# Optimization experiments

Hardware: AMD Instinct MI355X
Metric: run time of the kernel (lower is better)

## Reference

```python
import math
import jax, jax.numpy as jnp
import numpy as np

B, S, D, H, FF = 2, 2048, 1024, 16, 4096
DH = D // H
NUM_BUCKETS, MAX_DISTANCE = 32, 128
EPS_LN = 1e-5


def setup_inputs() -> dict:
    key = jax.random.key(0)
    ks = jax.random.split(key, 12)
    sc = 0.02
    return {
        "x": jax.random.normal(ks[0], (B, S, D), dtype=jnp.float32),
        "Wq": jax.random.normal(ks[1], (D, D), dtype=jnp.float32) * sc,
        "bq": jnp.zeros((D,), jnp.float32),
        "Wk": jax.random.normal(ks[2], (D, D), dtype=jnp.float32) * sc,
        "bk": jnp.zeros((D,), jnp.float32),
        "Wv": jax.random.normal(ks[3], (D, D), dtype=jnp.float32) * sc,
        "bv": jnp.zeros((D,), jnp.float32),
        "Wo": jax.random.normal(ks[4], (D, D), dtype=jnp.float32) * sc,
        "bo": jnp.zeros((D,), jnp.float32),
        "W1": jax.random.normal(ks[5], (D, FF), dtype=jnp.float32) * sc,
        "b1": jnp.zeros((FF,), jnp.float32),
        "W2": jax.random.normal(ks[6], (FF, D), dtype=jnp.float32) * sc,
        "b2": jnp.zeros((D,), jnp.float32),
        "g1": jnp.ones((D,), jnp.float32),
        "beta1": jnp.zeros((D,), jnp.float32),
        "g2": jnp.ones((D,), jnp.float32),
        "beta2": jnp.zeros((D,), jnp.float32),
        "rel_emb": jax.random.normal(ks[7], (NUM_BUCKETS, H), dtype=jnp.float32) * sc,
        "pad_mask": jnp.ones((B, 1, 1, S), dtype=jnp.bool_),
    }


def _rel_bias(rel_emb, qlen, klen):
    # T5 bidirectional relative position bucketing; n = q_pos - k_pos
    q = jnp.arange(qlen)[:, None]
    k = jnp.arange(klen)[None, :]
    n = q - k
    half = NUM_BUCKETS // 2           # 16
    ret = (n < 0).astype(jnp.int32) * half
    n_abs = jnp.abs(n)
    max_exact = half // 2             # 8
    log_ratio = math.log(MAX_DISTANCE / max_exact)
    val_large = (max_exact + jnp.log(n_abs.astype(jnp.float32) / max_exact + 1e-6)
                 / log_ratio * (half - max_exact)).astype(jnp.int32)
    val_large = jnp.minimum(val_large, half - 1)
    bucket = jnp.where(n_abs < max_exact, n_abs.astype(jnp.int32), val_large) + ret
    bias = rel_emb[bucket]            # [Q, K, H]
    return jnp.transpose(bias, (2, 0, 1))[None]  # [1, H, Q, K]


def _layernorm(x, g, b):
    mu = jnp.mean(x, axis=-1, keepdims=True)
    var = jnp.mean(jnp.square(x - mu), axis=-1, keepdims=True)
    return (x - mu) * jax.lax.rsqrt(var + EPS_LN) * g + b


def reference(x, Wq, bq, Wk, bk, Wv, bv, Wo, bo, W1, b1, W2, b2,
              g1, beta1, g2, beta2, rel_emb, pad_mask):
    b_, s_, d_ = x.shape
    rel = _rel_bias(rel_emb, s_, s_)
    h = _layernorm(x, g1, beta1)
    q = (h @ Wq + bq).reshape(b_, s_, H, DH)
    k = (h @ Wk + bk).reshape(b_, s_, H, DH)
    v = (h @ Wv + bv).reshape(b_, s_, H, DH)
    scores = jnp.einsum("bqhd,bkhd->bhqk", q, k) / math.sqrt(DH)
    scores = scores + rel
    scores = jnp.where(pad_mask, scores, jnp.finfo(scores.dtype).min)
    attn = jax.nn.softmax(scores, axis=-1)
    out = jnp.einsum("bhqk,bkhd->bqhd", attn, v).reshape(b_, s_, d_)
    x = x + (out @ Wo + bo)
    h2 = _layernorm(x, g2, beta2)
    ff = jax.nn.gelu(h2 @ W1 + b1, approximate=False) @ W2 + b2
    return x + ff
```

## Files before the change

kernel.cpp:

```cpp
#include <hip/hip_runtime.h>
#include <hip/hip_bf16.h>
#include <math.h>

#define S_LEN 2048
#define DMODEL 1024
#define NHEAD 16
#define FFDIM 4096
#define NTOK 4096
#define QKV_LD 3072

typedef __attribute__((ext_vector_type(8))) short bf16x8;
typedef __attribute__((ext_vector_type(4))) float f32x4;

static __device__ __forceinline__ unsigned short f2bf_bits(float f) {
    union { __hip_bfloat16 b; unsigned short u; } cv;
    cv.b = __float2bfloat16(f);
    return cv.u;
}

#define GLOAD16(src, dst) \
    __builtin_amdgcn_global_load_lds((const __attribute__((address_space(1))) void*)(src), \
                                     (__attribute__((address_space(3))) void*)(dst), 16, 0, 0)

__global__ __launch_bounds__(256) void transpose_bf16(
    const float* __restrict__ in, __hip_bfloat16* __restrict__ out, int R, int C)
{
    __shared__ float tile[32][33];
    const int c0 = blockIdx.x * 32, r0 = blockIdx.y * 32;
    const int tx = threadIdx.x & 31, ty = threadIdx.x >> 5;
#pragma unroll
    for (int i = 0; i < 4; i++) {
        int r = ty + i * 8;
        tile[r][tx] = in[(long)(r0 + r) * C + c0 + tx];
    }
    __syncthreads();
#pragma unroll
    for (int i = 0; i < 4; i++) {
        int c = ty + i * 8;
        out[(long)(c0 + c) * R + r0 + tx] = __float2bfloat16(tile[tx][c]);
    }
}

__global__ __launch_bounds__(256) void transpose_qkv_v(
    const __hip_bfloat16* __restrict__ in,
    __hip_bfloat16* __restrict__ out)
{
    __shared__ __hip_bfloat16 tile[32][33];
    const int bz = blockIdx.z;
    const int c0 = blockIdx.x * 32, r0 = blockIdx.y * 32;
    const int tx = threadIdx.x & 31, ty = threadIdx.x >> 5;
    const long ibase = (long)bz * S_LEN * QKV_LD;
#pragma unroll
    for (int i = 0; i < 4; i++) {
        int r = ty + i * 8;
        tile[r][tx] = in[ibase + (long)(r0 + r) * QKV_LD + c0 + tx];
    }
    __syncthreads();
    const long obase = (long)bz * DMODEL * S_LEN;
#pragma unroll
    for (int i = 0; i < 4; i++) {
        int c = ty + i * 8;
        out[obase + (long)(c0 + c) * S_LEN + r0 + tx] = tile[tx][c];
    }
}

__global__ __launch_bounds__(256) void biastab_kernel(
    const float* __restrict__ rel_emb, float* __restrict__ tab)
{
    int i = blockIdx.x * 256 + threadIdx.x;
    int h = i >> 12, idx = i & 4095;
    if (h >= NHEAD || idx >= 4095) return;
    int n = idx - 2047;
    int ret = (n < 0) ? 16 : 0;
    int na = (n < 0) ? -n : n;
    int bucket;
    if (na < 8) {
        bucket = na;
    } else {
        float vv = 8.0f + logf((float)na * 0.125f + 1e-6f) * (8.0f / 2.7725887222397811f);
        int vi = (int)vv;
        bucket = (vi < 15) ? vi : 15;
    }
    bucket += ret;
    tab[h * 4096 + idx] = rel_emb[bucket * NHEAD + h];
}

__global__ __launch_bounds__(256) void ln_bf16(
    const float* __restrict__ x, const float* __restrict__ gm,
    const float* __restrict__ bt, __hip_bfloat16* __restrict__ out)
{
    const long row = blockIdx.x;
    const int tid = threadIdx.x, w = tid >> 6;
    float4 v = ((const float4*)(x + row * DMODEL))[tid];
    float s = v.x + v.y + v.z + v.w;
#pragma unroll
    for (int m = 32; m >= 1; m >>= 1) s += __shfl_xor(s, m);
    __shared__ float red[4], red2[4];
    if ((tid & 63) == 0) red[w] = s;
    __syncthreads();
    float mu = (red[0] + red[1] + red[2] + red[3]) * (1.0f / DMODEL);
    float dx = v.x - mu, dy = v.y - mu, dz = v.z - mu, dw = v.w - mu;
    float s2 = dx * dx + dy * dy + dz * dz + dw * dw;
#pragma unroll
    for (int m = 32; m >= 1; m >>= 1) s2 += __shfl_xor(s2, m);
    if ((tid & 63) == 0) red2[w] = s2;
    __syncthreads();
    float var = (red2[0] + red2[1] + red2[2] + red2[3]) * (1.0f / DMODEL);
    float rs = rsqrtf(var + 1e-5f);
    float4 g4 = ((const float4*)gm)[tid];
    float4 b4 = ((const float4*)bt)[tid];
    long o = row * DMODEL + tid * 4;
    out[o + 0] = __float2bfloat16(dx * rs * g4.x + b4.x);
    out[o + 1] = __float2bfloat16(dy * rs * g4.y + b4.y);
    out[o + 2] = __float2bfloat16(dz * rs * g4.z + b4.z);
    out[o + 3] = __float2bfloat16(dw * rs * g4.w + b4.w);
}

template<int EPI>
__global__ __launch_bounds__(256) void gemm_bt(
    const __hip_bfloat16* __restrict__ A,
    const __hip_bfloat16* __restrict__ Bt,
    const float* __restrict__ bias,
    const float* __restrict__ resid,
    float* __restrict__ outf,
    __hip_bfloat16* __restrict__ outb,
    int K, int N)
{
    __shared__ __hip_bfloat16 As[2][128 * 32];
    __shared__ __hip_bfloat16 Bs[2][128 * 32];
    const int tid = threadIdx.x;
    const int lane = tid & 63, w = tid >> 6;
    const int cl = lane & 15, g = lane >> 4;
    const int wr = w >> 1, wc = w & 1;
    const int bm = blockIdx.x, bn = blockIdx.y;

    f32x4 acc[4][4] = {};

    const __hip_bfloat16* agp0 = A + (long)(bm * 128 + (tid >> 2)) * K + (tid & 3) * 8;
    const __hip_bfloat16* agp1 = agp0 + (long)64 * K;
    const __hip_bfloat16* bgp0 = Bt + (long)(bn * 128 + (tid >> 2)) * K + (tid & 3) * 8;
    const __hip_bfloat16* bgp1 = bgp0 + (long)64 * K;

    auto STAGE = [&](int buf, int k0) {
        GLOAD16(agp0 + k0, (char*)&As[buf][0] + w * 1024);
        GLOAD16(agp1 + k0, (char*)&As[buf][0] + 4096 + w * 1024);
        GLOAD16(bgp0 + k0, (char*)&Bs[buf][0] + w * 1024);
        GLOAD16(bgp1 + k0, (char*)&Bs[buf][0] + 4096 + w * 1024);
    };

    STAGE(0, 0);
    asm volatile("s_waitcnt vmcnt(0)" ::: "memory");
    __builtin_amdgcn_s_barrier();

    int cur = 0;
    for (int k0 = 0; k0 < K; k0 += 32) {
        if (k0 + 32 < K) STAGE(cur ^ 1, k0 + 32);
        bf16x8 af[4], bfv[4];
#pragma unroll
        for (int m = 0; m < 4; m++)
            af[m] = *reinterpret_cast<const bf16x8*>(&As[cur][(wr * 64 + m * 16 + cl) * 32 + g * 8]);
#pragma unroll
        for (int n = 0; n < 4; n++)
            bfv[n] = *reinterpret_cast<const bf16x8*>(&Bs[cur][(wc * 64 + n * 16 + cl) * 32 + g * 8]);
        __builtin_amdgcn_s_setprio(1);
#pragma unroll
        for (int m = 0; m < 4; m++)
#pragma unroll
            for (int n = 0; n < 4; n++)
                acc[m][n] = __builtin_amdgcn_mfma_f32_16x16x32_bf16(af[m], bfv[n], acc[m][n], 0, 0, 0);
        __builtin_amdgcn_s_setprio(0);
        asm volatile("s_waitcnt vmcnt(0)" ::: "memory");
        __builtin_amdgcn_s_barrier();
        cur ^= 1;
    }

#pragma unroll
    for (int m = 0; m < 4; m++) {
#pragma unroll
        for (int n = 0; n < 4; n++) {
#pragma unroll
            for (int r = 0; r < 4; r++) {
                int row = bm * 128 + wr * 64 + m * 16 + g * 4 + r;
                int col = bn * 128 + wc * 64 + n * 16 + cl;
                float vv = acc[m][n][r] + bias[col];
                long off = (long)row * N + col;
                if (EPI == 1) {
                    outf[off] = vv + resid[off];
                } else {
                    outb[off] = __float2bfloat16(vv);
                }
            }
        }
    }
}

template<int EPI>
__global__ __launch_bounds__(512, 2) void gemm256(
    const __hip_bfloat16* __restrict__ A,
    const __hip_bfloat16* __restrict__ Bt,
    const float* __restrict__ bias,
    const float* __restrict__ bias2,
    const float* __restrict__ bias3,
    __hip_bfloat16* __restrict__ outb,
    int K, int N)
{
    __shared__ char L[131072];
    const int tid = threadIdx.x, lane = tid & 63, w = tid >> 6;
    const int cl = lane & 15, g = lane >> 4;
    const int wm = w >> 2, wn = w & 3;
    const int nbn = N >> 8;
    const int nwg = 16 * nbn;
    const int bid = blockIdx.x;
    const int swz = (bid & 7) * (nwg >> 3) + (bid >> 3);
    const int bm = swz / nbn, bn = swz - bm * nbn;
    const int NT = K >> 6;

    f32x4 acc[8][4] = {};

    const int srow = tid >> 3;
    const int scol = ((tid & 7) ^ (srow & 7)) * 8;
    const __hip_bfloat16* Asrc = A  + (long)(bm * 256 + srow) * K + scol;
    const __hip_bfloat16* Bsrc = Bt + (long)(bn * 256 + srow) * K + scol;

    auto STAGE_A = [&](int buf, int half, int t) {
        const __hip_bfloat16* s = Asrc + (long)(half * 128) * K + t * 64;
        char* d = L + buf * 32768 + half * 16384 + w * 1024;
        GLOAD16(s, d);
        GLOAD16(s + (long)64 * K, d + 8192);
    };
    auto STAGE_B = [&](int buf, int half, int t) {
        const __hip_bfloat16* s = Bsrc + (long)(half * 128) * K + t * 64;
        char* d = L + 65536 + buf * 32768 + half * 16384 + w * 1024;
        GLOAD16(s, d);
        GLOAD16(s + (long)64 * K, d + 8192);
    };

    const char* arb = L + wm * 16384 + cl * 128;
    const char* brb = L + 65536 + (wn >> 1) * 16384 + (((wn & 1) * 64 + cl)) * 128;
    const int xo0 = (g * 16) ^ ((cl & 7) << 4);
    const int xo1 = (64 + g * 16) ^ ((cl & 7) << 4);

    STAGE_B(0, 0, 0); STAGE_B(0, 1, 0);
    STAGE_A(0, 0, 0); STAGE_A(0, 1, 0);
    STAGE_B(1, 0, 1); STAGE_B(1, 1, 1);
    asm volatile("s_waitcnt vmcnt(4)" ::: "memory");
    __builtin_amdgcn_s_barrier();

    bf16x8 bfr[4][2];
    for (int t2 = 0; t2 < NT; t2 += 2) {
        const bool more = (t2 + 2 < NT);
#pragma unroll
        for (int p = 0; p < 8; p++) {
            const int buf = p >> 2, mp = p & 3;
            const int bo = buf * 32768;
            if (mp == 0) {
#pragma unroll
                for (int n = 0; n < 4; n++) {
                    bfr[n][0] = *reinterpret_cast<const bf16x8*>(brb + bo + n * 2048 + xo0);
                    bfr[n][1] = *reinterpret_cast<const bf16x8*>(brb + bo + n * 2048 + xo1);
                }
            }
            bf16x8 a0k0 = *reinterpret_cast<const bf16x8*>(arb + bo + (mp * 2) * 2048 + xo0);
            bf16x8 a0k1 = *reinterpret_cast<const bf16x8*>(arb + bo + (mp * 2) * 2048 + xo1);
            bf16x8 a1k0 = *reinterpret_cast<const bf16x8*>(arb + bo + (mp * 2 + 1) * 2048 + xo0);
            bf16x8 a1k1 = *reinterpret_cast<const bf16x8*>(arb + bo + (mp * 2 + 1) * 2048 + xo1);
            if (p == 0)      { STAGE_A(1, 0, t2 + 1); }
            else if (p == 1) { STAGE_A(1, 1, t2 + 1); }
            else if (p == 2) { if (more) STAGE_B(0, 0, t2 + 2); }
            else if (p == 3) { if (more) STAGE_B(0, 1, t2 + 2); }
            else if (p == 4) { if (more) STAGE_A(0, 0, t2 + 2); }
            else if (p == 5) { if (more) STAGE_A(0, 1, t2 + 2); }
            else if (p == 6) { if (more) STAGE_B(1, 0, t2 + 3); }
            else             { if (more) STAGE_B(1, 1, t2 + 3); }
            __builtin_amdgcn_s_barrier();
            __builtin_amdgcn_s_setprio(1);
#pragma unroll
            for (int i = 0; i < 2; i++) {
                const int ma = mp * 2 + i;
                bf16x8 ak0 = i ? a1k0 : a0k0;
                bf16x8 ak1 = i ? a1k1 : a0k1;
#pragma unroll
                for (int n = 0; n < 4; n++) {
                    acc[ma][n] = __builtin_amdgcn_mfma_f32_16x16x32_bf16(ak0, bfr[n][0], acc[ma][n], 0, 0, 0);
                    acc[ma][n] = __builtin_amdgcn_mfma_f32_16x16x32_bf16(ak1, bfr[n][1], acc[ma][n], 0, 0, 0);
                }
            }
            __builtin_amdgcn_s_setprio(0);
            if (p == 3) {
                if (more) { asm volatile("s_waitcnt vmcnt(4)" ::: "memory"); }
                else      { asm volatile("s_waitcnt vmcnt(0)" ::: "memory"); }
            }
            if (p == 7) {
                if (more) { asm volatile("s_waitcnt vmcnt(4)" ::: "memory"); }
            }
            __builtin_amdgcn_s_barrier();
        }
    }

#pragma unroll
    for (int m = 0; m < 8; m++) {
#pragma unroll
        for (int n = 0; n < 4; n++) {
#pragma unroll
            for (int r = 0; r < 4; r++) {
                int row = bm * 256 + wm * 128 + m * 16 + g * 4 + r;
                int col = bn * 256 + wn * 64 + n * 16 + cl;
                long off = (long)row * N + col;
                if (EPI == 2) {
                    float vv = acc[m][n][r] + bias[col];
                    float ge = 0.5f * vv * (1.0f + erff(vv * 0.70710678118654752f));
                    outb[off] = __float2bfloat16(ge);
                } else {
                    const float* bp = (col < 1024) ? bias : ((col < 2048) ? bias2 : bias3);
                    float vv = acc[m][n][r] + bp[col & 1023];
                    outb[off] = __float2bfloat16(vv);
                }
            }
        }
    }
}

__global__ __launch_bounds__(512, 4) void attn_fwd(
    const __hip_bfloat16* __restrict__ qkv,
    const __hip_bfloat16* __restrict__ vt,
    const float* __restrict__ btab,
    __hip_bfloat16* __restrict__ out)
{
    __shared__ __hip_bfloat16 Ks[2][64 * 64];
    __shared__ __hip_bfloat16 Vs[2][64 * 64];
    __shared__ __hip_bfloat16 Pl[8][16 * 64];
    const int tid = threadIdx.x, lane = tid & 63, w = tid >> 6;
    const int cl = lane & 15, g = lane >> 4;
    const int swz = (blockIdx.x & 7) * 64 + (blockIdx.x >> 3);
    const int bh = swz >> 4, qblk = swz & 15;
    const int b = bh >> 4, h = bh & 15;
    const int q0 = qblk * 128;
    const long qbase = ((long)b * S_LEN) * QKV_LD + h * 64;
    const __hip_bfloat16* vbase = vt + (long)b * DMODEL * S_LEN + (long)(h * 64) * S_LEN;

    const int srow = tid >> 3, scol = (tid & 7) ^ (srow & 7);
    const __hip_bfloat16* kstage = qkv + qbase + 1024 + (long)srow * QKV_LD + scol * 8;
    const __hip_bfloat16* vstage = vbase + (long)srow * S_LEN + scol * 8;

    const int qrow_a = q0 + w * 16 + cl;
    bf16x8 aq[2];
    aq[0] = *reinterpret_cast<const bf16x8*>(qkv + qbase + (long)qrow_a * QKV_LD + g * 8);
    aq[1] = *reinterpret_cast<const bf16x8*>(qkv + qbase + (long)qrow_a * QKV_LD + 32 + g * 8);

    f32x4 accO[4] = {};
    float mrun[4], lrun[4];
#pragma unroll
    for (int r = 0; r < 4; r++) { mrun[r] = -INFINITY; lrun[r] = 0.0f; }

    const int qrow_c = q0 + w * 16 + g * 4;

    auto STAGE = [&](int buf, int kv) {
        GLOAD16(kstage + (long)kv * QKV_LD, (char*)&Ks[buf][0] + w * 1024);
        GLOAD16(vstage + kv, (char*)&Vs[buf][0] + w * 1024);
    };

    STAGE(0, 0);
    __syncthreads();
    int cur = 0;

    for (int kv0 = 0; kv0 < S_LEN; kv0 += 64) {
        if (kv0 + 64 < S_LEN) STAGE(cur ^ 1, kv0 + 64);
        f32x4 accS[4] = {};
#pragma unroll
        for (int nf = 0; nf < 4; nf++) {
            int row = nf * 16 + cl;
#pragma unroll
            for (int ks2 = 0; ks2 < 2; ks2++) {
                int bo = row * 128 + ((((ks2 * 4 + g)) ^ (row & 7)) << 4);
                bf16x8 bk = *reinterpret_cast<const bf16x8*>((const char*)&Ks[cur][0] + bo);
                accS[nf] = __builtin_amdgcn_mfma_f32_16x16x32_bf16(aq[ks2], bk, accS[nf], 0, 0, 0);
            }
        }
        float sc[4][4], pmax[4];
#pragma unroll
        for (int r = 0; r < 4; r++) pmax[r] = -INFINITY;
#pragma unroll
        for (int nf = 0; nf < 4; nf++) {
            int col = kv0 + nf * 16 + cl;
#pragma unroll
            for (int r = 0; r < 4; r++) {
                int row = qrow_c + r;
                float s = accS[nf][r] * 0.125f + btab[h * 4096 + (row - col + 2047)];
                sc[nf][r] = s;
                pmax[r] = fmaxf(pmax[r], s);
            }
        }
#pragma unroll
        for (int r = 0; r < 4; r++) {
            pmax[r] = fmaxf(pmax[r], __shfl_xor(pmax[r], 1));
            pmax[r] = fmaxf(pmax[r], __shfl_xor(pmax[r], 2));
            pmax[r] = fmaxf(pmax[r], __shfl_xor(pmax[r], 4));
            pmax[r] = fmaxf(pmax[r], __shfl_xor(pmax[r], 8));
        }
        float mnew[4], alpha[4], psum[4];
#pragma unroll
        for (int r = 0; r < 4; r++) {
            mnew[r] = fmaxf(mrun[r], pmax[r]);
            alpha[r] = __expf(mrun[r] - mnew[r]);
            psum[r] = 0.0f;
        }
#pragma unroll
        for (int nf = 0; nf < 4; nf++) {
#pragma unroll
            for (int r = 0; r < 4; r++) {
                float p = __expf(sc[nf][r] - mnew[r]);
                psum[r] += p;
                int row_l = g * 4 + r, col_l = nf * 16 + cl;
                int bo = ((row_l * 64 + col_l) * 2) ^ ((row_l & 7) << 4);
                *reinterpret_cast<unsigned short*>(reinterpret_cast<char*>(&Pl[w][0]) + bo) = f2bf_bits(p);
            }
        }
#pragma unroll
        for (int r = 0; r < 4; r++) {
            psum[r] += __shfl_xor(psum[r], 1);
            psum[r] += __shfl_xor(psum[r], 2);
            psum[r] += __shfl_xor(psum[r], 4);
            psum[r] += __shfl_xor(psum[r], 8);
            lrun[r] = lrun[r] * alpha[r] + psum[r];
            mrun[r] = mnew[r];
#pragma unroll
            for (int df = 0; df < 4; df++) accO[df][r] *= alpha[r];
        }
        asm volatile("s_waitcnt lgkmcnt(0)" ::: "memory");
        __builtin_amdgcn_sched_barrier(0);
#pragma unroll
        for (int ks2 = 0; ks2 < 2; ks2++) {
            int bo = ((cl * 64 + ks2 * 32 + g * 8) * 2) ^ ((cl & 7) << 4);
            bf16x8 ap = *reinterpret_cast<const bf16x8*>(reinterpret_cast<const char*>(&Pl[w][0]) + bo);
#pragma unroll
            for (int df = 0; df < 4; df++) {
                int row = df * 16 + cl;
                int bo2 = row * 128 + ((((ks2 * 4 + g)) ^ (row & 7)) << 4);
                bf16x8 bv = *reinterpret_cast<const bf16x8*>((const char*)&Vs[cur][0] + bo2);
                accO[df] = __builtin_amdgcn_mfma_f32_16x16x32_bf16(ap, bv, accO[df], 0, 0, 0);
            }
        }
        __syncthreads();
        cur ^= 1;
    }
#pragma unroll
    for (int df = 0; df < 4; df++) {
#pragma unroll
        for (int r = 0; r < 4; r++) {
            int row = qrow_c + r;
            int col = df * 16 + cl;
            out[((long)b * S_LEN + row) * DMODEL + h * 64 + col] = __float2bfloat16(accO[df][r] / lrun[r]);
        }
    }
}

extern "C" void kernel_launch(void* const* d_in, const int* in_sizes, int n_in,
                              void* d_out, int out_size, void* d_ws, size_t ws_size,
                              hipStream_t stream) {
    (void)in_sizes; (void)n_in; (void)out_size; (void)ws_size;
    const float* x   = (const float*)d_in[0];
    const float* Wq  = (const float*)d_in[1];
    const float* bq  = (const float*)d_in[2];
    const float* Wk  = (const float*)d_in[3];
    const float* bk  = (const float*)d_in[4];
    const float* Wv  = (const float*)d_in[5];
    const float* bv  = (const float*)d_in[6];
    const float* Wo  = (const float*)d_in[7];
    const float* bo  = (const float*)d_in[8];
    const float* W1  = (const float*)d_in[9];
    const float* b1  = (const float*)d_in[10];
    const float* W2  = (const float*)d_in[11];
    const float* b2  = (const float*)d_in[12];
    const float* g1  = (const float*)d_in[13];
    const float* be1 = (const float*)d_in[14];
    const float* g2  = (const float*)d_in[15];
    const float* be2 = (const float*)d_in[16];
    const float* rel = (const float*)d_in[17];
    float* outp = (float*)d_out;

    char* ws = (char*)d_ws;
    __hip_bfloat16* Wqkvt = (__hip_bfloat16*)(ws + ((size_t)0  << 20));
    __hip_bfloat16* Wot   = (__hip_bfloat16*)(ws + ((size_t)6  << 20));
    __hip_bfloat16* W1t   = (__hip_bfloat16*)(ws + ((size_t)8  << 20));
    __hip_bfloat16* W2t   = (__hip_bfloat16*)(ws + ((size_t)16 << 20));
    __hip_bfloat16* hb    = (__hip_bfloat16*)(ws + ((size_t)24 << 20));
    __hip_bfloat16* qkvb  = (__hip_bfloat16*)(ws + ((size_t)32 << 20));
    __hip_bfloat16* vtb   = (__hip_bfloat16*)(ws + ((size_t)56 << 20));
    __hip_bfloat16* ao    = (__hip_bfloat16*)(ws + ((size_t)64 << 20));
    float*          x2    = (float*)         (ws + ((size_t)72 << 20));
    __hip_bfloat16* h2b   = (__hip_bfloat16*)(ws + ((size_t)88 << 20));
    __hip_bfloat16* ffb   = (__hip_bfloat16*)(ws + ((size_t)24 << 20));
    float*          btb   = (float*)         (ws + ((size_t)96 << 20));

    dim3 blk(256);
    transpose_bf16<<<dim3(32, 32),  blk, 0, stream>>>(Wq, Wqkvt,                1024, 1024);
    transpose_bf16<<<dim3(32, 32),  blk, 0, stream>>>(Wk, Wqkvt + 1024 * 1024,  1024, 1024);
    transpose_bf16<<<dim3(32, 32),  blk, 0, stream>>>(Wv, Wqkvt + 2048 * 1024,  1024, 1024);
    transpose_bf16<<<dim3(32, 32),  blk, 0, stream>>>(Wo, Wot, 1024, 1024);
    transpose_bf16<<<dim3(128, 32), blk, 0, stream>>>(W1, W1t, 1024, 4096);
    transpose_bf16<<<dim3(32, 128), blk, 0, stream>>>(W2, W2t, 4096, 1024);
    biastab_kernel<<<dim3(256), blk, 0, stream>>>(rel, btb);
    ln_bf16<<<dim3(NTOK), blk, 0, stream>>>(x, g1, be1, hb);
    gemm256<3><<<dim3(192), dim3(512), 0, stream>>>(hb, Wqkvt, bq, bk, bv, qkvb, 1024, 3072);
    transpose_qkv_v<<<dim3(32, 64, 2), blk, 0, stream>>>(qkvb + 2048, vtb);
    attn_fwd<<<dim3(512), dim3(512), 0, stream>>>(qkvb, vtb, btb, ao);
    gemm_bt<1><<<dim3(32, 8), blk, 0, stream>>>(ao, Wot, bo, x, x2, nullptr, 1024, 1024);
    ln_bf16<<<dim3(NTOK), blk, 0, stream>>>(x2, g2, be2, h2b);
    gemm256<2><<<dim3(256), dim3(512), 0, stream>>>(h2b, W1t, b1, nullptr, nullptr, ffb, 1024, 4096);
    gemm_bt<1><<<dim3(32, 8), blk, 0, stream>>>(ffb, W2t, b2, x2, outp, nullptr, 4096, 1024);
}
```

Measured before the change: 456.5 us.

## Triple-buffer gemm_bt, stage attention bias in LDS, lazy softmax rescale, merge transposes

The gemm_bt kernel moves from double to triple buffering of its LDS tiles, prefetching two k-steps ahead and waiting only on the older loads. The attention kernel now copies its slice of the relative-bias table into shared memory once per block instead of gathering it from global memory for every score. Online-softmax rescaling is skipped unless the running max grows by more than a threshold, which cuts exp and multiply work but leaves larger unnormalised partial sums. The four square weight transposes are merged into a single launch to reduce launch overhead. The extra LDS in both kernels may lower occupancy.

```diff
diff --git a/kernel.cpp b/kernel.cpp
--- a/kernel.cpp
+++ b/kernel.cpp
@@ -21,6 +21,30 @@
 #define GLOAD16(src, dst) \
     __builtin_amdgcn_global_load_lds((const __attribute__((address_space(1))) void*)(src), \
                                      (__attribute__((address_space(3))) void*)(dst), 16, 0, 0)
+
+__global__ __launch_bounds__(256) void transpose_w4(
+    const float* __restrict__ Wq, const float* __restrict__ Wk,
+    const float* __restrict__ Wv, const float* __restrict__ Wo,
+    __hip_bfloat16* __restrict__ Wqkvt, __hip_bfloat16* __restrict__ Wot)
+{
+    __shared__ float tile[32][33];
+    const int z = blockIdx.z;
+    const float* in = (z == 0) ? Wq : (z == 1) ? Wk : (z == 2) ? Wv : Wo;
+    __hip_bfloat16* out = (z < 3) ? (Wqkvt + (size_t)z * 1024 * 1024) : Wot;
+    const int c0 = blockIdx.x * 32, r0 = blockIdx.y * 32;
+    const int tx = threadIdx.x & 31, ty = threadIdx.x >> 5;
+#pragma unroll
+    for (int i = 0; i < 4; i++) {
+        int r = ty + i * 8;
+        tile[r][tx] = in[(long)(r0 + r) * 1024 + c0 + tx];
+    }
+    __syncthreads();
+#pragma unroll
+    for (int i = 0; i < 4; i++) {
+        int c = ty + i * 8;
+        out[(long)(c0 + c) * 1024 + r0 + tx] = __float2bfloat16(tile[tx][c]);
+    }
+}
 
 __global__ __launch_bounds__(256) void transpose_bf16(
     const float* __restrict__ in, __hip_bfloat16* __restrict__ out, int R, int C)
@@ -117,7 +141,7 @@
 }
 
 template<int EPI>
-__global__ __launch_bounds__(256) void gemm_bt(
+__global__ __launch_bounds__(256, 3) void gemm_bt(
     const __hip_bfloat16* __restrict__ A,
     const __hip_bfloat16* __restrict__ Bt,
     const float* __restrict__ bias,
@@ -126,8 +150,8 @@
     __hip_bfloat16* __restrict__ outb,
     int K, int N)
 {
-    __shared__ __hip_bfloat16 As[2][128 * 32];
-    __shared__ __hip_bfloat16 Bs[2][128 * 32];
+    __shared__ __hip_bfloat16 As[3 * 128 * 32];
+    __shared__ __hip_bfloat16 Bs[3 * 128 * 32];
     const int tid = threadIdx.x;
     const int lane = tid & 63, w = tid >> 6;
     const int cl = lane & 15, g = lane >> 4;
@@ -142,26 +166,35 @@
     const __hip_bfloat16* bgp1 = bgp0 + (long)64 * K;
 
     auto STAGE = [&](int buf, int k0) {
-        GLOAD16(agp0 + k0, (char*)&As[buf][0] + w * 1024);
-        GLOAD16(agp1 + k0, (char*)&As[buf][0] + 4096 + w * 1024);
-        GLOAD16(bgp0 + k0, (char*)&Bs[buf][0] + w * 1024);
-        GLOAD16(bgp1 + k0, (char*)&Bs[buf][0] + 4096 + w * 1024);
+        char* ab = (char*)As + buf * 8192;
+        char* bb = (char*)Bs + buf * 8192;
+        GLOAD16(agp0 + k0, ab + w * 1024);
+        GLOAD16(agp1 + k0, ab + 4096 + w * 1024);
+        GLOAD16(bgp0 + k0, bb + w * 1024);
+        GLOAD16(bgp1 + k0, bb + 4096 + w * 1024);
     };
 
     STAGE(0, 0);
-    asm volatile("s_waitcnt vmcnt(0)" ::: "memory");
+    STAGE(1, 32);
+    asm volatile("s_waitcnt vmcnt(4)" ::: "memory");
     __builtin_amdgcn_s_barrier();
 
-    int cur = 0;
+    int bi = 0;
     for (int k0 = 0; k0 < K; k0 += 32) {
-        if (k0 + 32 < K) STAGE(cur ^ 1, k0 + 32);
+        const bool more = (k0 + 64 < K);
+        if (more) {
+            int nb = bi + 2; if (nb >= 3) nb -= 3;
+            STAGE(nb, k0 + 64);
+        }
+        const char* ab = (const char*)As + bi * 8192;
+        const char* bb = (const char*)Bs + bi * 8192;
         bf16x8 af[4], bfv[4];
 #pragma unroll
         for (int m = 0; m < 4; m++)
-            af[m] = *reinterpret_cast<const bf16x8*>(&As[cur][(wr * 64 + m * 16 + cl) * 32 + g * 8]);
+            af[m] = *reinterpret_cast<const bf16x8*>(ab + ((wr * 64 + m * 16 + cl) * 32 + g * 8) * 2);
 #pragma unroll
         for (int n = 0; n < 4; n++)
-            bfv[n] = *reinterpret_cast<const bf16x8*>(&Bs[cur][(wc * 64 + n * 16 + cl) * 32 + g * 8]);
+            bfv[n] = *reinterpret_cast<const bf16x8*>(bb + ((wc * 64 + n * 16 + cl) * 32 + g * 8) * 2);
         __builtin_amdgcn_s_setprio(1);
 #pragma unroll
         for (int m = 0; m < 4; m++)
@@ -169,9 +202,10 @@
             for (int n = 0; n < 4; n++)
                 acc[m][n] = __builtin_amdgcn_mfma_f32_16x16x32_bf16(af[m], bfv[n], acc[m][n], 0, 0, 0);
         __builtin_amdgcn_s_setprio(0);
-        asm volatile("s_waitcnt vmcnt(0)" ::: "memory");
+        if (more) { asm volatile("s_waitcnt vmcnt(4)" ::: "memory"); }
+        else      { asm volatile("s_waitcnt vmcnt(0)" ::: "memory"); }
         __builtin_amdgcn_s_barrier();
-        cur ^= 1;
+        bi = (bi == 2) ? 0 : bi + 1;
     }
 
 #pragma unroll
@@ -329,6 +363,7 @@
     __shared__ __hip_bfloat16 Ks[2][64 * 64];
     __shared__ __hip_bfloat16 Vs[2][64 * 64];
     __shared__ __hip_bfloat16 Pl[8][16 * 64];
+    __shared__ float Bl[2176];
     const int tid = threadIdx.x, lane = tid & 63, w = tid >> 6;
     const int cl = lane & 15, g = lane >> 4;
     const int swz = (blockIdx.x & 7) * 64 + (blockIdx.x >> 3);
@@ -360,8 +395,11 @@
     };
 
     STAGE(0, 0);
+    for (int i = tid; i < 2175; i += 512) Bl[i] = btab[h * 4096 + q0 + i];
     __syncthreads();
     int cur = 0;
+
+    const int ibl = w * 16 + g * 4 + 2047 - cl;
 
     for (int kv0 = 0; kv0 < S_LEN; kv0 += 64) {
         if (kv0 + 64 < S_LEN) STAGE(cur ^ 1, kv0 + 64);
@@ -381,11 +419,10 @@
         for (int r = 0; r < 4; r++) pmax[r] = -INFINITY;
 #pragma unroll
         for (int nf = 0; nf < 4; nf++) {
-            int col = kv0 + nf * 16 + cl;
+            int ib = ibl - kv0 - nf * 16;
 #pragma unroll
             for (int r = 0; r < 4; r++) {
-                int row = qrow_c + r;
-                float s = accS[nf][r] * 0.125f + btab[h * 4096 + (row - col + 2047)];
+                float s = accS[nf][r] * 0.125f + Bl[ib + r];
                 sc[nf][r] = s;
                 pmax[r] = fmaxf(pmax[r], s);
             }
@@ -397,18 +434,25 @@
             pmax[r] = fmaxf(pmax[r], __shfl_xor(pmax[r], 4));
             pmax[r] = fmaxf(pmax[r], __shfl_xor(pmax[r], 8));
         }
-        float mnew[4], alpha[4], psum[4];
-#pragma unroll
-        for (int r = 0; r < 4; r++) {
-            mnew[r] = fmaxf(mrun[r], pmax[r]);
-            alpha[r] = __expf(mrun[r] - mnew[r]);
-            psum[r] = 0.0f;
-        }
+        float grow = fmaxf(fmaxf(pmax[0] - mrun[0], pmax[1] - mrun[1]),
+                           fmaxf(pmax[2] - mrun[2], pmax[3] - mrun[3]));
+        if (!__all(grow <= 6.0f)) {
+#pragma unroll
+            for (int r = 0; r < 4; r++) {
+                float mnew = fmaxf(mrun[r], pmax[r]);
+                float alpha = __expf(mrun[r] - mnew);
+                lrun[r] *= alpha;
+#pragma unroll
+                for (int df = 0; df < 4; df++) accO[df][r] *= alpha;
+                mrun[r] = mnew;
+            }
+        }
+        float psum[4] = {};
 #pragma unroll
         for (int nf = 0; nf < 4; nf++) {
 #pragma unroll
             for (int r = 0; r < 4; r++) {
-                float p = __expf(sc[nf][r] - mnew[r]);
+                float p = __expf(sc[nf][r] - mrun[r]);
                 psum[r] += p;
                 int row_l = g * 4 + r, col_l = nf * 16 + cl;
                 int bo = ((row_l * 64 + col_l) * 2) ^ ((row_l & 7) << 4);
@@ -421,10 +465,7 @@
             psum[r] += __shfl_xor(psum[r], 2);
             psum[r] += __shfl_xor(psum[r], 4);
             psum[r] += __shfl_xor(psum[r], 8);
-            lrun[r] = lrun[r] * alpha[r] + psum[r];
-            mrun[r] = mnew[r];
-#pragma unroll
-            for (int df = 0; df < 4; df++) accO[df][r] *= alpha[r];
+            lrun[r] += psum[r];
         }
         asm volatile("s_waitcnt lgkmcnt(0)" ::: "memory");
         __builtin_amdgcn_sched_barrier(0);
@@ -493,10 +534,7 @@
     float*          btb   = (float*)         (ws + ((size_t)96 << 20));
 
     dim3 blk(256);
-    transpose_bf16<<<dim3(32, 32),  blk, 0, stream>>>(Wq, Wqkvt,                1024, 1024);
-    transpose_bf16<<<dim3(32, 32),  blk, 0, stream>>>(Wk, Wqkvt + 1024 * 1024,  1024, 1024);
-    transpose_bf16<<<dim3(32, 32),  blk, 0, stream>>>(Wv, Wqkvt + 2048 * 1024,  1024, 1024);
-    transpose_bf16<<<dim3(32, 32),  blk, 0, stream>>>(Wo, Wot, 1024, 1024);
+    transpose_w4<<<dim3(32, 32, 4), blk, 0, stream>>>(Wq, Wk, Wv, Wo, Wqkvt, Wot);
     transpose_bf16<<<dim3(128, 32), blk, 0, stream>>>(W1, W1t, 1024, 4096);
     transpose_bf16<<<dim3(32, 128), blk, 0, stream>>>(W2, W2t, 4096, 1024);
     biastab_kernel<<<dim3(256), blk, 0, stream>>>(rel, btb);
```

Result: no change. 455.5 us (-0.2%).
